# Kernel tuning notes

Hardware: AMD Instinct MI355X
Metric: run time of the kernel (lower is better)

The kernel has to match this reference:

```python
import jax, jax.numpy as jnp
import numpy as np

SCALE = 1.0 / np.sqrt(64.0)  # hard-coded 64**0.5 in original, independent of dims


def setup_inputs() -> dict:
    key = jax.random.key(0)
    k1, k2 = jax.random.split(key)
    x = jax.random.normal(k1, (8, 2048, 1024), dtype=jnp.float32)
    # kernel[0]=W_Q, kernel[1]=W_K, kernel[2]=W_V, each [d_in, d_out]
    kernel = jax.random.normal(k2, (3, 1024, 1024), dtype=jnp.float32) * 0.02
    return {"x": x, "kernel": kernel}


def reference(x, kernel):
    # x: [b, s, d_in], kernel: [3, d_in, d_out]
    wq = jnp.einsum('bsd,de->bse', x, kernel[0])
    wk = jnp.einsum('bsd,de->bse', x, kernel[1])
    wv = jnp.einsum('bsd,de->bse', x, kernel[2])
    scores = jnp.einsum('bqe,bke->bqk', wq, wk) * SCALE  # [b, s, s]
    attn = jax.nn.softmax(scores, axis=-1)
    return jnp.einsum('bqk,bke->bqe', attn, wv)  # [b, s, d_out]
```

## Files before the change

kernel.cpp:

```cpp
#include <hip/hip_runtime.h>
#include <stdint.h>

typedef unsigned short u16;
typedef unsigned short u16x8 __attribute__((ext_vector_type(8)));
typedef _Float16 f16x8 __attribute__((ext_vector_type(8)));
typedef float f32x4 __attribute__((ext_vector_type(4)));

__device__ __forceinline__ u16 f2h(float f) {
  _Float16 x = (_Float16)f;
  return __builtin_bit_cast(u16, x);
}
__device__ __forceinline__ float h2f(u16 h) {
  _Float16 x = __builtin_bit_cast(_Float16, h);
  return (float)x;
}

__device__ __forceinline__ void gld16(const void* g, void* l) {
  __builtin_amdgcn_global_load_lds(
      (const __attribute__((address_space(1))) unsigned int*)g,
      (__attribute__((address_space(3))) unsigned int*)l,
      16, 0, 0);
}

#define BAR __builtin_amdgcn_s_barrier()
#define SCHEDB __builtin_amdgcn_sched_barrier(0)
#define LGKM0                                        \
  do {                                               \
    asm volatile("s_waitcnt lgkmcnt(0)" ::: "memory"); \
    __builtin_amdgcn_sched_barrier(0);               \
  } while (0)
#define LGKM8 asm volatile("s_waitcnt lgkmcnt(8)" ::: "memory")
#define VM6 asm volatile("s_waitcnt vmcnt(6)" ::: "memory")
#define VM0 asm volatile("s_waitcnt vmcnt(0)" ::: "memory")

#define TBM 256
#define TBN 256
#define TBK 64

template <int QM, int QN>
__device__ __forceinline__ void mfma_quad(f32x4 (&acc)[8][4],
                                          const f16x8 (&ar)[4][2],
                                          const f16x8 (&br)[2][2]) {
#pragma unroll
  for (int kk = 0; kk < 2; ++kk)
#pragma unroll
    for (int mm = 0; mm < 4; ++mm)
#pragma unroll
      for (int nn = 0; nn < 2; ++nn)
        acc[QM * 4 + mm][QN * 2 + nn] = __builtin_amdgcn_mfma_f32_16x16x32_f16(
            ar[mm][kk], br[nn][kk], acc[QM * 4 + mm][QN * 2 + nn], 0, 0, 0);
}

template <int EPI, int XSWZ>
__global__ __launch_bounds__(512, 2) void gemm256(
    const u16* __restrict__ Ap, const u16* __restrict__ Bp,
    void* __restrict__ Cp, float* __restrict__ xtra, int K, int lda, int ldb,
    int ldc, long sA, long sB, long sC) {
  __shared__ char lds[131072];

  const int gx = gridDim.x, gy = gridDim.y;
  int bx, by, z;
  if constexpr (XSWZ == 1) {
    const int p = (blockIdx.z * gy + blockIdx.y) * gx + blockIdx.x;
    z = p & 7;
    const int rest = p >> 3;
    bx = rest % gx;
    by = rest / gx;
  } else {
    const int lin = (blockIdx.z * gy + blockIdx.y) * gx + blockIdx.x;
    const int cpx = (gx * gy * gridDim.z) >> 3;
    const int swz = (lin & 7) * cpx + (lin >> 3);
    bx = swz % gx;
    const int tq = swz / gx;
    by = tq % gy;
    z = tq / gy;
  }

  const int tid = threadIdx.x;
  const int lane = tid & 63, wid = tid >> 6;
  const int wr = wid >> 2, wc = wid & 3;
  const int l15 = lane & 15, l4 = lane >> 4;
  const int bm = by * TBM, bn = bx * TBN;

  const u16* Ag = Ap + (long)z * sA + (long)bm * lda;
  const u16* Bg = Bp + (long)z * sB + (long)bn * ldb;

  const int sw = l15 & 7;
  const int s0 = (l4 ^ sw) * 16, s1 = ((4 + l4) ^ sw) * 16;
  int aB[2][2], bB[2][2];
  aB[0][0] = wr * 16384 + l15 * 128 + s0;
  aB[0][1] = wr * 16384 + l15 * 128 + s1;
  bB[0][0] = 32768 + (wc >> 1) * 16384 + ((wc & 1) * 64 + l15) * 128 + s0;
  bB[0][1] = 32768 + (wc >> 1) * 16384 + ((wc & 1) * 64 + l15) * 128 + s1;
  aB[1][0] = aB[0][0] + 65536;
  aB[1][1] = aB[0][1] + 65536;
  bB[1][0] = bB[0][0] + 65536;
  bB[1][1] = bB[0][1] + 65536;

#define DSA(BUF, QM, AR)                                                     \
  do {                                                                       \
    _Pragma("unroll") for (int mm = 0; mm < 4; ++mm) {                       \
      AR[mm][0] = *(const f16x8*)(lds + aB[BUF][0] + (QM)*8192 + mm * 2048); \
      AR[mm][1] = *(const f16x8*)(lds + aB[BUF][1] + (QM)*8192 + mm * 2048); \
    }                                                                        \
  } while (0)
#define DSB(BUF, QN, BR)                                                     \
  do {                                                                       \
    _Pragma("unroll") for (int nn = 0; nn < 2; ++nn) {                       \
      BR[nn][0] = *(const f16x8*)(lds + bB[BUF][0] + (QN)*4096 + nn * 2048); \
      BR[nn][1] = *(const f16x8*)(lds + bB[BUF][1] + (QN)*4096 + nn * 2048); \
    }                                                                        \
  } while (0)

  const u16 *gpA0[2], *gpA1[2], *gpB0[2], *gpB1[2];
  int loA0[2], loA1[2], loB0[2], loB1[2];
  {
    const u16* bases[4] = {Ag, Ag + 128L * lda, Bg, Bg + 128L * ldb};
    const int lds_[4] = {lda, lda, ldb, ldb};
    const u16** gps[4] = {gpA0, gpA1, gpB0, gpB1};
    int* los[4] = {loA0, loA1, loB0, loB1};
#pragma unroll
    for (int X = 0; X < 4; ++X)
#pragma unroll
      for (int it = 0; it < 2; ++it) {
        int idx = it * 512 + tid, r = idx >> 3, p = idx & 7, s = p ^ (r & 7);
        gps[X][it] = bases[X] + (long)r * lds_[X] + s * 8;
        los[X][it] = X * 16384 + (it * 512 + wid * 64) * 16;
      }
  }
#define STAGE(X, BUF, kt)                                            \
  do {                                                               \
    long ko = (long)(kt) << 7;                                       \
    gld16((const char*)gp##X[0] + ko, lds + ((BUF)*65536 + lo##X[0])); \
    gld16((const char*)gp##X[1] + ko, lds + ((BUF)*65536 + lo##X[1])); \
  } while (0)

  f32x4 acc[8][4] = {};
  f16x8 a0[4][2], a1[4][2], b0[2][2], b1[2][2];
  const int nk = K / TBK;

  STAGE(A0, 0, 0);
  STAGE(A1, 0, 0);
  STAGE(B0, 0, 0);
  STAGE(B1, 0, 0);
  STAGE(A0, 1, 1);
  STAGE(A1, 1, 1);
  STAGE(B0, 1, 1);
  VM6;
  BAR;
  SCHEDB;

#define TILE(BUF, t)                                              \
  do {                                                            \
                    \
    DSA(BUF, 0, a0);                                              \
    DSB(BUF, 0, b0);                                              \
    if ((t) + 1 < nk) STAGE(B1, BUF ^ 1, (t) + 1);                \
    LGKM8;                                                        \
    BAR;                                                          \
    LGKM0;                                                        \
    __builtin_amdgcn_s_setprio(1);                                \
    mfma_quad<0, 0>(acc, a0, b0);                                 \
    __builtin_amdgcn_s_setprio(0);                                \
    SCHEDB;                                                       \
    BAR;                                                          \
                        \
    DSA(BUF, 1, a1);                                              \
    if ((t) + 2 < nk) STAGE(A0, BUF, (t) + 2);                    \
    BAR;                                                          \
    LGKM0;                                                        \
    __builtin_amdgcn_s_setprio(1);                                \
    mfma_quad<1, 0>(acc, a1, b0);                                 \
    __builtin_amdgcn_s_setprio(0);                                \
    SCHEDB;                                                       \
    BAR;                                                          \
                        \
    DSB(BUF, 1, b1);                                              \
    if ((t) + 2 < nk) STAGE(A1, BUF, (t) + 2);                    \
    BAR;                                                          \
    LGKM0;                                                        \
    __builtin_amdgcn_s_setprio(1);                                \
    mfma_quad<0, 1>(acc, a0, b1);                                 \
    __builtin_amdgcn_s_setprio(0);                                \
    SCHEDB;                                                       \
    BAR;                                                          \
     \
    if ((t) + 2 < nk) {                                           \
      STAGE(B0, BUF, (t) + 2);                                    \
      VM6;                                                        \
    } else if ((t) + 1 < nk) {                                    \
      VM0;                                                        \
    }                                                             \
    BAR;                                                          \
    __builtin_amdgcn_s_setprio(1);                                \
    mfma_quad<1, 1>(acc, a1, b1);                                 \
    __builtin_amdgcn_s_setprio(0);                                \
    SCHEDB;                                                       \
    BAR;                                                          \
  } while (0)

  for (int t = 0; t < nk; t += 2) {
    TILE(0, t);
    TILE(1, t + 1);
  }

  if constexpr (EPI == 0) {
    u16* C = (u16*)Cp + (long)z * sC;
#pragma unroll
    for (int m = 0; m < 8; ++m)
#pragma unroll
      for (int n = 0; n < 4; ++n) {
        int row = bm + wr * 128 + m * 16 + l4 * 4;
        int col = bn + wc * 64 + n * 16 + l15;
#pragma unroll
        for (int r = 0; r < 4; ++r)
          C[(long)(row + r) * ldc + col] = f2h(acc[m][n][r]);
      }
  } else if constexpr (EPI == 1) {
    u16* C = (u16*)Cp + (long)z * sC;
    float* rp = (float*)lds;
#pragma unroll
    for (int m = 0; m < 8; ++m) {
#pragma unroll
      for (int r = 0; r < 4; ++r) {
        const int row = bm + wr * 128 + m * 16 + l4 * 4 + r;
        float ps = 0.f;
#pragma unroll
        for (int n = 0; n < 4; ++n) {
          float p = __expf(acc[m][n][r] * 0.125f - 3.0f);
          C[(long)row * ldc + bn + wc * 64 + n * 16 + l15] = f2h(p);
          ps += p;
        }
#pragma unroll
        for (int d = 1; d < 16; d <<= 1) ps += __shfl_xor(ps, d, 64);
        if (l15 == 0) rp[wc * 256 + wr * 128 + m * 16 + l4 * 4 + r] = ps;
      }
    }
    __syncthreads();
    if (tid < 256) {
      float s = rp[tid] + rp[256 + tid] + rp[512 + tid] + rp[768 + tid];
      xtra[((long)z * 2048 + bm + tid) * 8 + bx] = s;
    }
  } else {
    float* C = (float*)Cp + (long)z * sC;
#pragma unroll
    for (int m = 0; m < 8; ++m)
#pragma unroll
      for (int r = 0; r < 4; ++r) {
        const int row = bm + wr * 128 + m * 16 + l4 * 4 + r;
        const float iv = xtra[(long)z * 2048 + row];
#pragma unroll
        for (int n = 0; n < 4; ++n)
          C[(long)row * ldc + bn + wc * 64 + n * 16 + l15] =
              acc[m][n][r] * iv;
      }
  }
#undef TILE
#undef STAGE
#undef DSA
#undef DSB
}

__global__ __launch_bounds__(256) void rowinv_k(const float* __restrict__ Spart,
                                                float* __restrict__ rowinv) {
  const int i = blockIdx.x * 256 + threadIdx.x;
  const float* p = Spart + (long)i * 8;
  float s = 0.f;
#pragma unroll
  for (int j = 0; j < 8; ++j) s += p[j];
  rowinv[i] = 1.0f / s;
}

template <typename TIN>
__global__ __launch_bounds__(256) void transpose_to_f16(
    const TIN* __restrict__ in, u16* __restrict__ out, int R, int C, int ldin,
    long sIn, long sOut) {
  __shared__ u16 T[64][72];
  const long bi = blockIdx.z;
  const TIN* ip = in + bi * sIn;
  u16* op = out + bi * sOut;
  const int r0 = blockIdx.y * 64, c0 = blockIdx.x * 64;
  const int t = threadIdx.x, c8 = t & 7, rr = t >> 3;
#pragma unroll
  for (int h = 0; h < 2; ++h) {
    const int r = rr + h * 32;
    u16x8 v;
    if constexpr (sizeof(TIN) == 4) {
      const float* g = (const float*)ip + (long)(r0 + r) * ldin + c0 + c8 * 8;
      float4 a = *(const float4*)g;
      float4 b = *(const float4*)(g + 4);
      v[0] = f2h(a.x); v[1] = f2h(a.y); v[2] = f2h(a.z); v[3] = f2h(a.w);
      v[4] = f2h(b.x); v[5] = f2h(b.y); v[6] = f2h(b.z); v[7] = f2h(b.w);
    } else {
      v = *(const u16x8*)((const u16*)ip + (long)(r0 + r) * ldin + c0 + c8 * 8);
    }
    *(u16x8*)&T[r][c8 * 8] = v;
  }
  __syncthreads();
#pragma unroll
  for (int h = 0; h < 2; ++h) {
    const int oc = rr + h * 32;
    u16x8 v;
#pragma unroll
    for (int j = 0; j < 8; ++j) v[j] = T[c8 * 8 + j][oc];
    *(u16x8*)(op + (long)(c0 + oc) * R + r0 + c8 * 8) = v;
  }
}

__global__ __launch_bounds__(256) void f32_to_f16(const float* __restrict__ in,
                                                  u16* __restrict__ out,
                                                  long n8) {
  long i = (long)blockIdx.x * 256 + threadIdx.x;
  const long stride = (long)gridDim.x * 256;
  for (; i < n8; i += stride) {
    const float* g = in + i * 8;
    float4 a = *(const float4*)g;
    float4 b = *(const float4*)(g + 4);
    u16x8 o;
    o[0] = f2h(a.x); o[1] = f2h(a.y); o[2] = f2h(a.z); o[3] = f2h(a.w);
    o[4] = f2h(b.x); o[5] = f2h(b.y); o[6] = f2h(b.z); o[7] = f2h(b.w);
    *(u16x8*)(out + i * 8) = o;
  }
}

extern "C" void kernel_launch(void* const* d_in, const int* in_sizes, int n_in,
                              void* d_out, int out_size, void* d_ws,
                              size_t ws_size, hipStream_t stream) {
  const float* x = (const float*)d_in[0];
  const float* w = (const float*)d_in[1];
  float* out = (float*)d_out;

  u16* ws = (u16*)d_ws;
  u16* QKV = ws;
  u16* Wt = ws + 50331648L;
  float* Spart = (float*)(ws + 50331648L);
  float* rowinv = (float*)(ws + 50593792L);
  u16* Vt = ws + 53477376L;
  u16* xh = ws + 70254592L;
  u16* S = ws + 70254592L;

  f32_to_f16<<<2048, 256, 0, stream>>>(x, xh, 2097152L);

  transpose_to_f16<float><<<dim3(16, 16, 3), 256, 0, stream>>>(
      w, Wt, 1024, 1024, 1024, 1048576L, 1048576L);

  gemm256<0, 0><<<dim3(12, 64, 1), 512, 0, stream>>>(
      xh, Wt, (void*)QKV, nullptr, 1024, 1024, 1024, 3072, 0L, 0L, 0L);

  transpose_to_f16<u16><<<dim3(16, 32, 8), 256, 0, stream>>>(
      QKV + 2048, Vt, 2048, 1024, 3072, 6291456L, 2097152L);

  gemm256<1, 1><<<dim3(8, 8, 8), 512, 0, stream>>>(
      QKV, QKV + 1024, (void*)S, Spart, 1024, 3072, 3072, 2048, 6291456L,
      6291456L, 4194304L);

  rowinv_k<<<dim3(64), 256, 0, stream>>>(Spart, rowinv);

  gemm256<2, 1><<<dim3(4, 8, 8), 512, 0, stream>>>(
      S, Vt, (void*)out, rowinv, 2048, 2048, 2048, 1024, 4194304L, 2097152L,
      2097152L);
}
```

Before: 287.1 us.

## Switch GEMMs to 32x32x16 MFMA and fuse V transpose into projection epilogue

Replaces the 16x16x32 MFMA tiling with 32x32x16 MFMA instructions, reorganizing the LDS read pattern and accumulator layout. The aim is fewer LDS fragment reads and instructions per FLOP. The QKV projection epilogue now writes V directly in transposed layout, removing the separate transpose kernel and its extra memory pass. The PV epilogue also caches row-inverse factors in LDS. Risks include higher register pressure and strided, partially coalesced stores in the transposed V write.

```diff
diff --git a/kernel.cpp b/kernel.cpp
--- a/kernel.cpp
+++ b/kernel.cpp
@@ -2,9 +2,10 @@
 #include <stdint.h>
 
 typedef unsigned short u16;
+typedef unsigned short u16x4 __attribute__((ext_vector_type(4)));
 typedef unsigned short u16x8 __attribute__((ext_vector_type(8)));
 typedef _Float16 f16x8 __attribute__((ext_vector_type(8)));
-typedef float f32x4 __attribute__((ext_vector_type(4)));
+typedef float f32x16 __attribute__((ext_vector_type(16)));
 
 __device__ __forceinline__ u16 f2h(float f) {
   _Float16 x = (_Float16)f;
@@ -38,17 +39,15 @@
 #define TBK 64
 
 template <int QM, int QN>
-__device__ __forceinline__ void mfma_quad(f32x4 (&acc)[8][4],
-                                          const f16x8 (&ar)[4][2],
-                                          const f16x8 (&br)[2][2]) {
-#pragma unroll
-  for (int kk = 0; kk < 2; ++kk)
-#pragma unroll
-    for (int mm = 0; mm < 4; ++mm)
-#pragma unroll
-      for (int nn = 0; nn < 2; ++nn)
-        acc[QM * 4 + mm][QN * 2 + nn] = __builtin_amdgcn_mfma_f32_16x16x32_f16(
-            ar[mm][kk], br[nn][kk], acc[QM * 4 + mm][QN * 2 + nn], 0, 0, 0);
+__device__ __forceinline__ void mfma_quad(f32x16 (&acc)[4][2],
+                                          const f16x8 (&ar)[2][4],
+                                          const f16x8 (&br)[4]) {
+#pragma unroll
+  for (int kk = 0; kk < 4; ++kk)
+#pragma unroll
+    for (int mm = 0; mm < 2; ++mm)
+      acc[QM * 2 + mm][QN] = __builtin_amdgcn_mfma_f32_32x32x16_f16(
+          ar[mm][kk], br[kk], acc[QM * 2 + mm][QN], 0, 0, 0);
 }
 
 template <int EPI, int XSWZ>
@@ -79,37 +78,31 @@
   const int tid = threadIdx.x;
   const int lane = tid & 63, wid = tid >> 6;
   const int wr = wid >> 2, wc = wid & 3;
-  const int l15 = lane & 15, l4 = lane >> 4;
+  const int l31 = lane & 31, h5 = lane >> 5;
   const int bm = by * TBM, bn = bx * TBN;
 
   const u16* Ag = Ap + (long)z * sA + (long)bm * lda;
   const u16* Bg = Bp + (long)z * sB + (long)bn * ldb;
 
-  const int sw = l15 & 7;
-  const int s0 = (l4 ^ sw) * 16, s1 = ((4 + l4) ^ sw) * 16;
-  int aB[2][2], bB[2][2];
-  aB[0][0] = wr * 16384 + l15 * 128 + s0;
-  aB[0][1] = wr * 16384 + l15 * 128 + s1;
-  bB[0][0] = 32768 + (wc >> 1) * 16384 + ((wc & 1) * 64 + l15) * 128 + s0;
-  bB[0][1] = 32768 + (wc >> 1) * 16384 + ((wc & 1) * 64 + l15) * 128 + s1;
-  aB[1][0] = aB[0][0] + 65536;
-  aB[1][1] = aB[0][1] + 65536;
-  bB[1][0] = bB[0][0] + 65536;
-  bB[1][1] = bB[0][1] + 65536;
-
-#define DSA(BUF, QM, AR)                                                     \
-  do {                                                                       \
-    _Pragma("unroll") for (int mm = 0; mm < 4; ++mm) {                       \
-      AR[mm][0] = *(const f16x8*)(lds + aB[BUF][0] + (QM)*8192 + mm * 2048); \
-      AR[mm][1] = *(const f16x8*)(lds + aB[BUF][1] + (QM)*8192 + mm * 2048); \
-    }                                                                        \
-  } while (0)
-#define DSB(BUF, QN, BR)                                                     \
-  do {                                                                       \
-    _Pragma("unroll") for (int nn = 0; nn < 2; ++nn) {                       \
-      BR[nn][0] = *(const f16x8*)(lds + bB[BUF][0] + (QN)*4096 + nn * 2048); \
-      BR[nn][1] = *(const f16x8*)(lds + bB[BUF][1] + (QN)*4096 + nn * 2048); \
-    }                                                                        \
+  int slt[4];
+#pragma unroll
+  for (int kk = 0; kk < 4; ++kk)
+    slt[kk] = (((kk << 1) | h5) ^ (lane & 7)) << 4;
+  const int pA = wr * 16384 + l31 * 128;
+  const int pB = 32768 + (wc >> 1) * 16384 + ((wc & 1) * 64 + l31) * 128;
+
+#define DSA(BUF, QM, AR)                                                    \
+  do {                                                                      \
+    _Pragma("unroll") for (int mm = 0; mm < 2; ++mm)                        \
+        _Pragma("unroll") for (int kk = 0; kk < 4; ++kk)                    \
+            AR[mm][kk] = *(const f16x8*)(lds + (BUF)*65536 + pA +           \
+                                         ((QM)*2 + mm) * 4096 + slt[kk]);   \
+  } while (0)
+#define DSB(BUF, QN, BR)                                                    \
+  do {                                                                      \
+    _Pragma("unroll") for (int kk = 0; kk < 4; ++kk)                        \
+        BR[kk] = *(const f16x8*)(lds + (BUF)*65536 + pB + (QN)*4096 +       \
+                                 slt[kk]);                                  \
   } while (0)
 
   const u16 *gpA0[2], *gpA1[2], *gpB0[2], *gpB1[2];
@@ -128,15 +121,15 @@
         los[X][it] = X * 16384 + (it * 512 + wid * 64) * 16;
       }
   }
-#define STAGE(X, BUF, kt)                                            \
-  do {                                                               \
-    long ko = (long)(kt) << 7;                                       \
+#define STAGE(X, BUF, kt)                                              \
+  do {                                                                 \
+    long ko = (long)(kt) << 7;                                         \
     gld16((const char*)gp##X[0] + ko, lds + ((BUF)*65536 + lo##X[0])); \
     gld16((const char*)gp##X[1] + ko, lds + ((BUF)*65536 + lo##X[1])); \
   } while (0)
 
-  f32x4 acc[8][4] = {};
-  f16x8 a0[4][2], a1[4][2], b0[2][2], b1[2][2];
+  f32x16 acc[4][2] = {};
+  f16x8 a0[2][4], a1[2][4], b0[4], b1[4];
   const int nk = K / TBK;
 
   STAGE(A0, 0, 0);
@@ -150,53 +143,53 @@
   BAR;
   SCHEDB;
 
-#define TILE(BUF, t)                                              \
-  do {                                                            \
-                    \
-    DSA(BUF, 0, a0);                                              \
-    DSB(BUF, 0, b0);                                              \
-    if ((t) + 1 < nk) STAGE(B1, BUF ^ 1, (t) + 1);                \
-    LGKM8;                                                        \
-    BAR;                                                          \
-    LGKM0;                                                        \
-    __builtin_amdgcn_s_setprio(1);                                \
-    mfma_quad<0, 0>(acc, a0, b0);                                 \
-    __builtin_amdgcn_s_setprio(0);                                \
-    SCHEDB;                                                       \
-    BAR;                                                          \
-                        \
-    DSA(BUF, 1, a1);                                              \
-    if ((t) + 2 < nk) STAGE(A0, BUF, (t) + 2);                    \
-    BAR;                                                          \
-    LGKM0;                                                        \
-    __builtin_amdgcn_s_setprio(1);                                \
-    mfma_quad<1, 0>(acc, a1, b0);                                 \
-    __builtin_amdgcn_s_setprio(0);                                \
-    SCHEDB;                                                       \
-    BAR;                                                          \
-                        \
-    DSB(BUF, 1, b1);                                              \
-    if ((t) + 2 < nk) STAGE(A1, BUF, (t) + 2);                    \
-    BAR;                                                          \
-    LGKM0;                                                        \
-    __builtin_amdgcn_s_setprio(1);                                \
-    mfma_quad<0, 1>(acc, a0, b1);                                 \
-    __builtin_amdgcn_s_setprio(0);                                \
-    SCHEDB;                                                       \
-    BAR;                                                          \
+#define TILE(BUF, t)                                                 \
+  do {                                                               \
+                       \
+    DSA(BUF, 0, a0);                                                 \
+    DSB(BUF, 0, b0);                                                 \
+    if ((t) + 1 < nk) STAGE(B1, BUF ^ 1, (t) + 1);                   \
+    LGKM8;                                                           \
+    BAR;                                                             \
+    LGKM0;                                                           \
+    __builtin_amdgcn_s_setprio(1);                                   \
+    mfma_quad<0, 0>(acc, a0, b0);                                    \
+    __builtin_amdgcn_s_setprio(0);                                   \
+    SCHEDB;                                                          \
+    BAR;                                                             \
+                           \
+    DSA(BUF, 1, a1);                                                 \
+    if ((t) + 2 < nk) STAGE(A0, BUF, (t) + 2);                       \
+    BAR;                                                             \
+    LGKM0;                                                           \
+    __builtin_amdgcn_s_setprio(1);                                   \
+    mfma_quad<1, 0>(acc, a1, b0);                                    \
+    __builtin_amdgcn_s_setprio(0);                                   \
+    SCHEDB;                                                          \
+    BAR;                                                             \
+                           \
+    DSB(BUF, 1, b1);                                                 \
+    if ((t) + 2 < nk) STAGE(A1, BUF, (t) + 2);                       \
+    BAR;                                                             \
+    LGKM0;                                                           \
+    __builtin_amdgcn_s_setprio(1);                                   \
+    mfma_quad<0, 1>(acc, a0, b1);                                    \
+    __builtin_amdgcn_s_setprio(0);                                   \
+    SCHEDB;                                                          \
+    BAR;                                                             \
      \
-    if ((t) + 2 < nk) {                                           \
-      STAGE(B0, BUF, (t) + 2);                                    \
-      VM6;                                                        \
-    } else if ((t) + 1 < nk) {                                    \
-      VM0;                                                        \
-    }                                                             \
-    BAR;                                                          \
-    __builtin_amdgcn_s_setprio(1);                                \
-    mfma_quad<1, 1>(acc, a1, b1);                                 \
-    __builtin_amdgcn_s_setprio(0);                                \
-    SCHEDB;                                                       \
-    BAR;                                                          \
+    if ((t) + 2 < nk) {                                              \
+      STAGE(B0, BUF, (t) + 2);                                       \
+      VM6;                                                           \
+    } else if ((t) + 1 < nk) {                                       \
+      VM0;                                                           \
+    }                                                                \
+    BAR;                                                             \
+    __builtin_amdgcn_s_setprio(1);                                   \
+    mfma_quad<1, 1>(acc, a1, b1);                                    \
+    __builtin_amdgcn_s_setprio(0);                                   \
+    SCHEDB;                                                          \
+    BAR;                                                             \
   } while (0)
 
   for (int t = 0; t < nk; t += 2) {
@@ -205,35 +198,72 @@
   }
 
   if constexpr (EPI == 0) {
-    u16* C = (u16*)Cp + (long)z * sC;
-#pragma unroll
-    for (int m = 0; m < 8; ++m)
-#pragma unroll
-      for (int n = 0; n < 4; ++n) {
-        int row = bm + wr * 128 + m * 16 + l4 * 4;
-        int col = bn + wc * 64 + n * 16 + l15;
-#pragma unroll
-        for (int r = 0; r < 4; ++r)
-          C[(long)(row + r) * ldc + col] = f2h(acc[m][n][r]);
-      }
+    if (bn < 2048) {
+      u16* C = (u16*)Cp;
+#pragma unroll
+      for (int mf = 0; mf < 4; ++mf)
+#pragma unroll
+        for (int nf = 0; nf < 2; ++nf) {
+          const int rowb = bm + wr * 128 + mf * 32 + 4 * h5;
+          const int col = bn + wc * 64 + nf * 32 + l31;
+#pragma unroll
+          for (int g = 0; g < 4; ++g)
+#pragma unroll
+            for (int rr = 0; rr < 4; ++rr)
+              C[(long)(rowb + g * 8 + rr) * ldc + col] =
+                  f2h(acc[mf][nf][g * 4 + rr]);
+        }
+    } else {
+      u16* Vt = (u16*)xtra;
+#pragma unroll
+      for (int mf = 0; mf < 4; ++mf)
+#pragma unroll
+        for (int nf = 0; nf < 2; ++nf) {
+          const int rowb = bm + wr * 128 + mf * 32 + 4 * h5;
+          const int e = (bn - 2048) + wc * 64 + nf * 32 + l31;
+          const int zz = rowb >> 11, k0 = rowb & 2047;
+          u16* dst = Vt + (long)zz * 2097152 + (long)e * 2048 + k0;
+#pragma unroll
+          for (int g = 0; g < 4; ++g) {
+            u16x4 pk;
+#pragma unroll
+            for (int rr = 0; rr < 4; ++rr)
+              pk[rr] = f2h(acc[mf][nf][g * 4 + rr]);
+            *(u16x4*)(dst + g * 8) = pk;
+          }
+        }
+    }
   } else if constexpr (EPI == 1) {
     u16* C = (u16*)Cp + (long)z * sC;
     float* rp = (float*)lds;
 #pragma unroll
-    for (int m = 0; m < 8; ++m) {
-#pragma unroll
-      for (int r = 0; r < 4; ++r) {
-        const int row = bm + wr * 128 + m * 16 + l4 * 4 + r;
-        float ps = 0.f;
-#pragma unroll
-        for (int n = 0; n < 4; ++n) {
-          float p = __expf(acc[m][n][r] * 0.125f - 3.0f);
-          C[(long)row * ldc + bn + wc * 64 + n * 16 + l15] = f2h(p);
-          ps += p;
-        }
-#pragma unroll
-        for (int d = 1; d < 16; d <<= 1) ps += __shfl_xor(ps, d, 64);
-        if (l15 == 0) rp[wc * 256 + wr * 128 + m * 16 + l4 * 4 + r] = ps;
+    for (int mf = 0; mf < 4; ++mf) {
+      float rs[16];
+#pragma unroll
+      for (int reg = 0; reg < 16; ++reg) rs[reg] = 0.f;
+      const int rowb = bm + wr * 128 + mf * 32 + 4 * h5;
+#pragma unroll
+      for (int nf = 0; nf < 2; ++nf) {
+        const int col = bn + wc * 64 + nf * 32 + l31;
+#pragma unroll
+        for (int g = 0; g < 4; ++g)
+#pragma unroll
+          for (int rr = 0; rr < 4; ++rr) {
+            float p = __expf(acc[mf][nf][g * 4 + rr] * 0.125f - 3.0f);
+            C[(long)(rowb + g * 8 + rr) * ldc + col] = f2h(p);
+            rs[g * 4 + rr] += p;
+          }
+      }
+#pragma unroll
+      for (int reg = 0; reg < 16; ++reg)
+#pragma unroll
+        for (int d = 1; d < 32; d <<= 1)
+          rs[reg] += __shfl_xor(rs[reg], d, 64);
+      if (l31 == 0) {
+#pragma unroll
+        for (int reg = 0; reg < 16; ++reg)
+          rp[wc * 256 + wr * 128 + mf * 32 + (reg & 3) + 8 * (reg >> 2) +
+             4 * h5] = rs[reg];
       }
     }
     __syncthreads();
@@ -243,17 +273,24 @@
     }
   } else {
     float* C = (float*)Cp + (long)z * sC;
-#pragma unroll
-    for (int m = 0; m < 8; ++m)
-#pragma unroll
-      for (int r = 0; r < 4; ++r) {
-        const int row = bm + wr * 128 + m * 16 + l4 * 4 + r;
-        const float iv = xtra[(long)z * 2048 + row];
-#pragma unroll
-        for (int n = 0; n < 4; ++n)
-          C[(long)row * ldc + bn + wc * 64 + n * 16 + l15] =
-              acc[m][n][r] * iv;
-      }
+    float* ivl = (float*)lds;
+    if (tid < 256) ivl[tid] = xtra[(long)z * 2048 + bm + tid];
+    __syncthreads();
+#pragma unroll
+    for (int mf = 0; mf < 4; ++mf) {
+      const int rloc = wr * 128 + mf * 32 + 4 * h5;
+#pragma unroll
+      for (int g = 0; g < 4; ++g)
+#pragma unroll
+        for (int rr = 0; rr < 4; ++rr) {
+          const float iv = ivl[rloc + g * 8 + rr];
+          const long row = bm + rloc + g * 8 + rr;
+#pragma unroll
+          for (int nf = 0; nf < 2; ++nf)
+            C[row * ldc + bn + wc * 64 + nf * 32 + l31] =
+                acc[mf][nf][g * 4 + rr] * iv;
+        }
+    }
   }
 #undef TILE
 #undef STAGE
@@ -271,29 +308,24 @@
   rowinv[i] = 1.0f / s;
 }
 
-template <typename TIN>
-__global__ __launch_bounds__(256) void transpose_to_f16(
-    const TIN* __restrict__ in, u16* __restrict__ out, int R, int C, int ldin,
-    long sIn, long sOut) {
+__global__ __launch_bounds__(256) void transpose_f32_to_f16(
+    const float* __restrict__ in, u16* __restrict__ out, int R, int C,
+    int ldin, long sIn, long sOut) {
   __shared__ u16 T[64][72];
   const long bi = blockIdx.z;
-  const TIN* ip = in + bi * sIn;
+  const float* ip = in + bi * sIn;
   u16* op = out + bi * sOut;
   const int r0 = blockIdx.y * 64, c0 = blockIdx.x * 64;
   const int t = threadIdx.x, c8 = t & 7, rr = t >> 3;
 #pragma unroll
   for (int h = 0; h < 2; ++h) {
     const int r = rr + h * 32;
+    const float* g = ip + (long)(r0 + r) * ldin + c0 + c8 * 8;
+    float4 a = *(const float4*)g;
+    float4 b = *(const float4*)(g + 4);
     u16x8 v;
-    if constexpr (sizeof(TIN) == 4) {
-      const float* g = (const float*)ip + (long)(r0 + r) * ldin + c0 + c8 * 8;
-      float4 a = *(const float4*)g;
-      float4 b = *(const float4*)(g + 4);
-      v[0] = f2h(a.x); v[1] = f2h(a.y); v[2] = f2h(a.z); v[3] = f2h(a.w);
-      v[4] = f2h(b.x); v[5] = f2h(b.y); v[6] = f2h(b.z); v[7] = f2h(b.w);
-    } else {
-      v = *(const u16x8*)((const u16*)ip + (long)(r0 + r) * ldin + c0 + c8 * 8);
-    }
+    v[0] = f2h(a.x); v[1] = f2h(a.y); v[2] = f2h(a.z); v[3] = f2h(a.w);
+    v[4] = f2h(b.x); v[5] = f2h(b.y); v[6] = f2h(b.z); v[7] = f2h(b.w);
     *(u16x8*)&T[r][c8 * 8] = v;
   }
   __syncthreads();
@@ -341,14 +373,11 @@
 
   f32_to_f16<<<2048, 256, 0, stream>>>(x, xh, 2097152L);
 
-  transpose_to_f16<float><<<dim3(16, 16, 3), 256, 0, stream>>>(
+  transpose_f32_to_f16<<<dim3(16, 16, 3), 256, 0, stream>>>(
       w, Wt, 1024, 1024, 1024, 1048576L, 1048576L);
 
   gemm256<0, 0><<<dim3(12, 64, 1), 512, 0, stream>>>(
-      xh, Wt, (void*)QKV, nullptr, 1024, 1024, 1024, 3072, 0L, 0L, 0L);
-
-  transpose_to_f16<u16><<<dim3(16, 32, 8), 256, 0, stream>>>(
-      QKV + 2048, Vt, 2048, 1024, 3072, 6291456L, 2097152L);
+      xh, Wt, (void*)QKV, (float*)Vt, 1024, 1024, 1024, 3072, 0L, 0L, 0L);
 
   gemm256<1, 1><<<dim3(8, 8, 8), 512, 0, stream>>>(
       QKV, QKV + 1024, (void*)S, Spart, 1024, 3072, 3072, 2048, 6291456L,
```

After: 328.9 us. 1.15x slower.

## Fuse V transpose into QKV GEMM epilogue via swizzled LDS staging

Applied to the files above, without the earlier changes.

The QKV projection GEMM epilogue now writes V column blocks straight to a transposed Vt buffer, staging through swizzled LDS, so the separate V transpose kernel and its extra read/write pass over V are gone. Q and K blocks still store normally. The final GEMM epilogue also loads its row-inverse scale factors into LDS once per block instead of each thread reading them from global memory. In exchange the GEMM epilogue gains an LDS round trip and a barrier for the V blocks.

```diff
diff --git a/kernel.cpp b/kernel.cpp
--- a/kernel.cpp
+++ b/kernel.cpp
@@ -2,6 +2,7 @@
 #include <stdint.h>
 
 typedef unsigned short u16;
+typedef unsigned short u16x4 __attribute__((ext_vector_type(4)));
 typedef unsigned short u16x8 __attribute__((ext_vector_type(8)));
 typedef _Float16 f16x8 __attribute__((ext_vector_type(8)));
 typedef float f32x4 __attribute__((ext_vector_type(4)));
@@ -9,10 +10,6 @@
 __device__ __forceinline__ u16 f2h(float f) {
   _Float16 x = (_Float16)f;
   return __builtin_bit_cast(u16, x);
-}
-__device__ __forceinline__ float h2f(u16 h) {
-  _Float16 x = __builtin_bit_cast(_Float16, h);
-  return (float)x;
 }
 
 __device__ __forceinline__ void gld16(const void* g, void* l) {
@@ -128,9 +125,9 @@
         los[X][it] = X * 16384 + (it * 512 + wid * 64) * 16;
       }
   }
-#define STAGE(X, BUF, kt)                                            \
-  do {                                                               \
-    long ko = (long)(kt) << 7;                                       \
+#define STAGE(X, BUF, kt)                                              \
+  do {                                                                 \
+    long ko = (long)(kt) << 7;                                         \
     gld16((const char*)gp##X[0] + ko, lds + ((BUF)*65536 + lo##X[0])); \
     gld16((const char*)gp##X[1] + ko, lds + ((BUF)*65536 + lo##X[1])); \
   } while (0)
@@ -150,53 +147,53 @@
   BAR;
   SCHEDB;
 
-#define TILE(BUF, t)                                              \
-  do {                                                            \
-                    \
-    DSA(BUF, 0, a0);                                              \
-    DSB(BUF, 0, b0);                                              \
-    if ((t) + 1 < nk) STAGE(B1, BUF ^ 1, (t) + 1);                \
-    LGKM8;                                                        \
-    BAR;                                                          \
-    LGKM0;                                                        \
-    __builtin_amdgcn_s_setprio(1);                                \
-    mfma_quad<0, 0>(acc, a0, b0);                                 \
-    __builtin_amdgcn_s_setprio(0);                                \
-    SCHEDB;                                                       \
-    BAR;                                                          \
-                        \
-    DSA(BUF, 1, a1);                                              \
-    if ((t) + 2 < nk) STAGE(A0, BUF, (t) + 2);                    \
-    BAR;                                                          \
-    LGKM0;                                                        \
-    __builtin_amdgcn_s_setprio(1);                                \
-    mfma_quad<1, 0>(acc, a1, b0);                                 \
-    __builtin_amdgcn_s_setprio(0);                                \
-    SCHEDB;                                                       \
-    BAR;                                                          \
-                        \
-    DSB(BUF, 1, b1);                                              \
-    if ((t) + 2 < nk) STAGE(A1, BUF, (t) + 2);                    \
-    BAR;                                                          \
-    LGKM0;                                                        \
-    __builtin_amdgcn_s_setprio(1);                                \
-    mfma_quad<0, 1>(acc, a0, b1);                                 \
-    __builtin_amdgcn_s_setprio(0);                                \
-    SCHEDB;                                                       \
-    BAR;                                                          \
+#define TILE(BUF, t)                                                 \
+  do {                                                               \
+                       \
+    DSA(BUF, 0, a0);                                                 \
+    DSB(BUF, 0, b0);                                                 \
+    if ((t) + 1 < nk) STAGE(B1, BUF ^ 1, (t) + 1);                   \
+    LGKM8;                                                           \
+    BAR;                                                             \
+    LGKM0;                                                           \
+    __builtin_amdgcn_s_setprio(1);                                   \
+    mfma_quad<0, 0>(acc, a0, b0);                                    \
+    __builtin_amdgcn_s_setprio(0);                                   \
+    SCHEDB;                                                          \
+    BAR;                                                             \
+                           \
+    DSA(BUF, 1, a1);                                                 \
+    if ((t) + 2 < nk) STAGE(A0, BUF, (t) + 2);                       \
+    BAR;                                                             \
+    LGKM0;                                                           \
+    __builtin_amdgcn_s_setprio(1);                                   \
+    mfma_quad<1, 0>(acc, a1, b0);                                    \
+    __builtin_amdgcn_s_setprio(0);                                   \
+    SCHEDB;                                                          \
+    BAR;                                                             \
+                           \
+    DSB(BUF, 1, b1);                                                 \
+    if ((t) + 2 < nk) STAGE(A1, BUF, (t) + 2);                       \
+    BAR;                                                             \
+    LGKM0;                                                           \
+    __builtin_amdgcn_s_setprio(1);                                   \
+    mfma_quad<0, 1>(acc, a0, b1);                                    \
+    __builtin_amdgcn_s_setprio(0);                                   \
+    SCHEDB;                                                          \
+    BAR;                                                             \
      \
-    if ((t) + 2 < nk) {                                           \
-      STAGE(B0, BUF, (t) + 2);                                    \
-      VM6;                                                        \
-    } else if ((t) + 1 < nk) {                                    \
-      VM0;                                                        \
-    }                                                             \
-    BAR;                                                          \
-    __builtin_amdgcn_s_setprio(1);                                \
-    mfma_quad<1, 1>(acc, a1, b1);                                 \
-    __builtin_amdgcn_s_setprio(0);                                \
-    SCHEDB;                                                       \
-    BAR;                                                          \
+    if ((t) + 2 < nk) {                                              \
+      STAGE(B0, BUF, (t) + 2);                                       \
+      VM6;                                                           \
+    } else if ((t) + 1 < nk) {                                       \
+      VM0;                                                           \
+    }                                                                \
+    BAR;                                                             \
+    __builtin_amdgcn_s_setprio(1);                                   \
+    mfma_quad<1, 1>(acc, a1, b1);                                    \
+    __builtin_amdgcn_s_setprio(0);                                   \
+    SCHEDB;                                                          \
+    BAR;                                                             \
   } while (0)
 
   for (int t = 0; t < nk; t += 2) {
@@ -205,17 +202,48 @@
   }
 
   if constexpr (EPI == 0) {
-    u16* C = (u16*)Cp + (long)z * sC;
-#pragma unroll
-    for (int m = 0; m < 8; ++m)
-#pragma unroll
-      for (int n = 0; n < 4; ++n) {
-        int row = bm + wr * 128 + m * 16 + l4 * 4;
-        int col = bn + wc * 64 + n * 16 + l15;
-#pragma unroll
-        for (int r = 0; r < 4; ++r)
-          C[(long)(row + r) * ldc + col] = f2h(acc[m][n][r]);
-      }
+    if (bn < 2048) {
+      u16* C = (u16*)Cp;
+#pragma unroll
+      for (int m = 0; m < 8; ++m)
+#pragma unroll
+        for (int n = 0; n < 4; ++n) {
+          int row = bm + wr * 128 + m * 16 + l4 * 4;
+          int col = bn + wc * 64 + n * 16 + l15;
+#pragma unroll
+          for (int r = 0; r < 4; ++r)
+            C[(long)(row + r) * ldc + col] = f2h(acc[m][n][r]);
+        }
+    } else {
+#pragma unroll
+      for (int m = 0; m < 8; ++m) {
+        const int slotk = wr * 16 + m * 2 + (l4 >> 1);
+        const int koff8 = (l4 & 1) * 8;
+#pragma unroll
+        for (int n = 0; n < 4; ++n) {
+          const int e = wc * 64 + n * 16 + l15;
+          u16x4 pk;
+#pragma unroll
+          for (int rr = 0; rr < 4; ++rr) pk[rr] = f2h(acc[m][n][rr]);
+          *(u16x4*)(lds + e * 512 + ((slotk ^ (e & 31)) << 4) + koff8) = pk;
+        }
+      }
+      __syncthreads();
+      u16* Vt = (u16*)xtra;
+      const int zz = bm >> 11;
+      const int kb = bm & 2047;
+      const int e = tid >> 1;
+      const int c2 = (tid & 1) * 16;
+      u16* dst = Vt + (long)zz * 2097152 + (long)((bn - 2048) + e) * 2048 + kb;
+      const char* src = lds + e * 512;
+      const int ex = e & 31;
+#pragma unroll
+      for (int j = 0; j < 16; ++j) {
+        const int c = c2 + j;
+        u16x8 v = *(const u16x8*)(src + ((c ^ ex) << 4));
+        *(u16x8*)(dst + c * 8) = v;
+      }
+    }
   } else if constexpr (EPI == 1) {
     u16* C = (u16*)Cp + (long)z * sC;
     float* rp = (float*)lds;
@@ -243,16 +271,19 @@
     }
   } else {
     float* C = (float*)Cp + (long)z * sC;
+    float* ivl = (float*)lds;
+    if (tid < 256) ivl[tid] = xtra[(long)z * 2048 + bm + tid];
+    __syncthreads();
 #pragma unroll
     for (int m = 0; m < 8; ++m)
 #pragma unroll
       for (int r = 0; r < 4; ++r) {
-        const int row = bm + wr * 128 + m * 16 + l4 * 4 + r;
-        const float iv = xtra[(long)z * 2048 + row];
+        const int rloc = wr * 128 + m * 16 + l4 * 4 + r;
+        const float iv = ivl[rloc];
+        const long row = bm + rloc;
 #pragma unroll
         for (int n = 0; n < 4; ++n)
-          C[(long)row * ldc + bn + wc * 64 + n * 16 + l15] =
-              acc[m][n][r] * iv;
+          C[row * ldc + bn + wc * 64 + n * 16 + l15] = acc[m][n][r] * iv;
       }
   }
 #undef TILE
@@ -271,29 +302,24 @@
   rowinv[i] = 1.0f / s;
 }
 
-template <typename TIN>
-__global__ __launch_bounds__(256) void transpose_to_f16(
-    const TIN* __restrict__ in, u16* __restrict__ out, int R, int C, int ldin,
-    long sIn, long sOut) {
+__global__ __launch_bounds__(256) void transpose_f32_to_f16(
+    const float* __restrict__ in, u16* __restrict__ out, int R, int C,
+    int ldin, long sIn, long sOut) {
   __shared__ u16 T[64][72];
   const long bi = blockIdx.z;
-  const TIN* ip = in + bi * sIn;
+  const float* ip = in + bi * sIn;
   u16* op = out + bi * sOut;
   const int r0 = blockIdx.y * 64, c0 = blockIdx.x * 64;
   const int t = threadIdx.x, c8 = t & 7, rr = t >> 3;
 #pragma unroll
   for (int h = 0; h < 2; ++h) {
     const int r = rr + h * 32;
+    const float* g = ip + (long)(r0 + r) * ldin + c0 + c8 * 8;
+    float4 a = *(const float4*)g;
+    float4 b = *(const float4*)(g + 4);
     u16x8 v;
-    if constexpr (sizeof(TIN) == 4) {
-      const float* g = (const float*)ip + (long)(r0 + r) * ldin + c0 + c8 * 8;
-      float4 a = *(const float4*)g;
-      float4 b = *(const float4*)(g + 4);
-      v[0] = f2h(a.x); v[1] = f2h(a.y); v[2] = f2h(a.z); v[3] = f2h(a.w);
-      v[4] = f2h(b.x); v[5] = f2h(b.y); v[6] = f2h(b.z); v[7] = f2h(b.w);
-    } else {
-      v = *(const u16x8*)((const u16*)ip + (long)(r0 + r) * ldin + c0 + c8 * 8);
-    }
+    v[0] = f2h(a.x); v[1] = f2h(a.y); v[2] = f2h(a.z); v[3] = f2h(a.w);
+    v[4] = f2h(b.x); v[5] = f2h(b.y); v[6] = f2h(b.z); v[7] = f2h(b.w);
     *(u16x8*)&T[r][c8 * 8] = v;
   }
   __syncthreads();
@@ -341,14 +367,11 @@
 
   f32_to_f16<<<2048, 256, 0, stream>>>(x, xh, 2097152L);
 
-  transpose_to_f16<float><<<dim3(16, 16, 3), 256, 0, stream>>>(
+  transpose_f32_to_f16<<<dim3(16, 16, 3), 256, 0, stream>>>(
       w, Wt, 1024, 1024, 1024, 1048576L, 1048576L);
 
   gemm256<0, 0><<<dim3(12, 64, 1), 512, 0, stream>>>(
-      xh, Wt, (void*)QKV, nullptr, 1024, 1024, 1024, 3072, 0L, 0L, 0L);
-
-  transpose_to_f16<u16><<<dim3(16, 32, 8), 256, 0, stream>>>(
-      QKV + 2048, Vt, 2048, 1024, 3072, 6291456L, 2097152L);
+      xh, Wt, (void*)QKV, (float*)Vt, 1024, 1024, 1024, 3072, 0L, 0L, 0L);
 
   gemm256<1, 1><<<dim3(8, 8, 8), 512, 0, stream>>>(
       QKV, QKV + 1024, (void*)S, Spart, 1024, 3072, 3072, 2048, 6291456L,
```

Measured after the change: 280.4 us. -2.3%, faster.
